# Kernel optimization log

Hardware: AMD Instinct MI355X
Metric: run time of the kernel (lower is better)

The kernel has to match this reference:

```python
import jax, jax.numpy as jnp
import numpy as np

NEG_SLOPE = 0.2  # PyG GATv2Conv default


def with_self_loops(edge_index, n):
    loop = jnp.arange(n, dtype=edge_index.dtype)
    src = jnp.concatenate([edge_index[0], loop])
    dst = jnp.concatenate([edge_index[1], loop])
    return src, dst


def gatv2(x, src, dst, Wl, bl, Wr, br, att, bias):
    """PyG GATv2Conv (eval mode, concat=True, add_self_loops done by caller).
    x: [N, F_in]; att: [H, C]. Returns [N, H*C]."""
    N = x.shape[0]
    H, C = att.shape
    xl = (x @ Wl + bl).reshape(N, H, C)  # lin_l(x): source-side transform
    xr = (x @ Wr + br).reshape(N, H, C)  # lin_r(x): target-side transform
    s = jax.nn.leaky_relu(xl[src] + xr[dst], NEG_SLOPE)      # [E,H,C]
    logit = jnp.einsum('ehc,hc->eh', s, att)                 # [E,H]
    m = jax.ops.segment_max(logit, dst, num_segments=N)      # stable softmax per target
    e = jnp.exp(logit - m[dst])
    den = jax.ops.segment_sum(e, dst, num_segments=N)
    alpha = e / (den[dst] + 1e-16)                           # [E,H]
    out = jax.ops.segment_sum(alpha[:, :, None] * xl[src], dst, num_segments=N)
    return out.reshape(N, H * C) + bias


def setup_inputs() -> dict:
    N, E = 20000, 320000        # agent nodes / edges
    M, EM = 40000, 400000       # lane nodes / edges
    B, L = 64, 50               # focal agents, centerline length
    SEQ, INC, HID, HEADS, OUT = 50, 2, 32, 4, 60
    H4 = HID * HEADS
    key = jax.random.key(0)
    ks = list(jax.random.split(key, 48))
    kit = iter(ks)

    def p(shape):
        return jax.random.normal(next(kit), shape, jnp.float32) * 0.05

    inp = {
        'x': jax.random.normal(next(kit), (N, SEQ, INC), jnp.float32),
        'edge_index': jax.random.randint(next(kit), (2, E), 0, N),
        'lane_x': jax.random.normal(next(kit), (M, 2), jnp.float32),
        'lane_edge_index': jax.random.randint(next(kit), (2, EM), 0, M),
        'batch': jnp.sort(jax.random.randint(next(kit), (N,), 0, B)),
        'focal_idx': jax.random.randint(next(kit), (B,), 0, N),
        'centerlines': jax.random.normal(next(kit), (B, L, 2), jnp.float32),
        # agent embedding
        'ae_W': p((SEQ * INC, HID)), 'ae_b': p((HID,)),
        # agent subgraph conv1 / conv2
        'a1_Wl': p((HID, H4)), 'a1_bl': p((H4,)), 'a1_Wr': p((HID, H4)), 'a1_br': p((H4,)), 'a1_att': p((HEADS, HID)), 'a1_b': p((H4,)),
        'a2_Wl': p((H4, H4)), 'a2_bl': p((H4,)), 'a2_Wr': p((H4, H4)), 'a2_br': p((H4,)), 'a2_att': p((HEADS, HID)), 'a2_b': p((H4,)),
        # map embedding + map subgraph
        'me_W': p((2, HID)), 'me_b': p((HID,)),
        'm1_Wl': p((HID, H4)), 'm1_bl': p((H4,)), 'm1_Wr': p((HID, H4)), 'm1_br': p((H4,)), 'm1_att': p((HEADS, HID)), 'm1_b': p((H4,)),
        'm2_Wl': p((H4, H4)), 'm2_bl': p((H4,)), 'm2_Wr': p((H4, H4)), 'm2_br': p((H4,)), 'm2_att': p((HEADS, HID)), 'm2_b': p((H4,)),
        # centerline processor
        'cl_W': p((2, HID)), 'cl_b': p((HID,)),
        # global graph (heads=1)
        'g_Wl': p((H4, HID)), 'g_bl': p((HID,)), 'g_Wr': p((H4, HID)), 'g_br': p((HID,)), 'g_att': p((1, HID)), 'g_b': p((HID,)),
        # output head
        'fc_W': p((2 * HID, OUT)), 'fc_b': p((OUT,)),
    }
    return inp


def reference(x, edge_index, lane_x, lane_edge_index, batch, focal_idx, centerlines,
              ae_W, ae_b,
              a1_Wl, a1_bl, a1_Wr, a1_br, a1_att, a1_b,
              a2_Wl, a2_bl, a2_Wr, a2_br, a2_att, a2_b,
              me_W, me_b,
              m1_Wl, m1_bl, m1_Wr, m1_br, m1_att, m1_b,
              m2_Wl, m2_bl, m2_Wr, m2_br, m2_att, m2_b,
              cl_W, cl_b,
              g_Wl, g_bl, g_Wr, g_br, g_att, g_b,
              fc_W, fc_b):
    N = x.shape[0]
    M = lane_x.shape[0]
    # agent branch
    agent_x = jax.nn.relu(x.reshape(N, -1) @ ae_W + ae_b)
    a_src, a_dst = with_self_loops(edge_index, N)
    h = jax.nn.relu(gatv2(agent_x, a_src, a_dst, a1_Wl, a1_bl, a1_Wr, a1_br, a1_att, a1_b))
    agent_features = jax.nn.relu(gatv2(h, a_src, a_dst, a2_Wl, a2_bl, a2_Wr, a2_br, a2_att, a2_b))  # [N,128]
    # map branch (output unused downstream in original, computed for faithfulness)
    map_x = jax.nn.relu(lane_x @ me_W + me_b)
    m_src, m_dst = with_self_loops(lane_edge_index, M)
    hm = jax.nn.relu(gatv2(map_x, m_src, m_dst, m1_Wl, m1_bl, m1_Wr, m1_br, m1_att, m1_b))
    map_features = jax.nn.relu(gatv2(hm, m_src, m_dst, m2_Wl, m2_bl, m2_Wr, m2_br, m2_att, m2_b))
    _ = map_features  # global_mean_pool results are dead code in the original forward
    # global graph over agent features (heads=1)
    global_features = jax.nn.relu(gatv2(agent_features, a_src, a_dst, g_Wl, g_bl, g_Wr, g_br, g_att, g_b))  # [N,32]
    focal = global_features[focal_idx]  # [B,32]
    # centerlines: per-polyline mean then linear (no relu, as in original)
    cl_feat = jnp.mean(centerlines, axis=1) @ cl_W + cl_b  # [B,32]
    combined = jnp.concatenate([focal, cl_feat], axis=1)
    return combined @ fc_W + fc_b
```

## Files before the change

### kernel.cpp

```cpp
#include <hip/hip_runtime.h>
#include <hip/hip_bf16.h>
#include <hip/hip_fp16.h>
#include <math.h>

typedef __hip_bfloat16 bf16;
#define NEG_SLOPE 0.2f

typedef _Float16 f16x8 __attribute__((ext_vector_type(8)));
typedef float f32x4 __attribute__((ext_vector_type(4)));

__global__ void k_detect_zero(const unsigned short* __restrict__ x, int* __restrict__ flag,
                              int* __restrict__ zbase, int n) {
    for (int i = blockIdx.x * blockDim.x + threadIdx.x; i < n; i += gridDim.x * blockDim.x)
        zbase[i] = 0;
    if (blockIdx.x == 0) {
        __shared__ int cnt;
        if (threadIdx.x == 0) cnt = 0;
        __syncthreads();
        int local = 0;
        for (int i = threadIdx.x; i < 2048; i += blockDim.x) {
            unsigned short w = x[2 * i];
            int e = (w >> 7) & 0xFF;
            if (e >= 0x90) local++;
        }
        atomicAdd(&cnt, local);
        __syncthreads();
        if (threadIdx.x == 0) flag[0] = (cnt > 100) ? 1 : 0;
    }
}

#define NSEG 25
struct Seg { const void* src; int n; int off; };
struct Tab { Seg s[NSEG]; };

__device__ __forceinline__ float ldconv(const void* src, int i, int f32mode) {
    return f32mode ? ((const float*)src)[i]
                   : __bfloat162float(((const bf16*)src)[i]);
}

__global__ void k_convert(Tab tab, float* __restrict__ dst, const int* __restrict__ flag,
                          const int* __restrict__ dstArr, int E, int N,
                          int* __restrict__ deg, int* __restrict__ rank,
                          const void* a2WlS, const void* a2WrS,
                          const void* gWlS, const void* gWrS,
                          __half* __restrict__ a2Wlt, __half* __restrict__ a2Wrt,
                          __half* __restrict__ gWlt, __half* __restrict__ gWrt) {
    int f32mode = flag[0];
    int gid = blockIdx.x * blockDim.x + threadIdx.x;
    int gsz = gridDim.x * blockDim.x;
    for (int s = 0; s < NSEG; s++) {
        Seg sg = tab.s[s];
        for (int i = gid; i < sg.n; i += gsz) {
            dst[sg.off + i] = ldconv(sg.src, i, f32mode);
        }
    }
    for (int i = gid; i < 128 * 128; i += gsz) {
        int k = i >> 7, j = i & 127;
        a2Wlt[(size_t)j * 128 + k] = __float2half(ldconv(a2WlS, i, f32mode));
        a2Wrt[(size_t)j * 128 + k] = __float2half(ldconv(a2WrS, i, f32mode));
    }
    for (int i = gid; i < 128 * 32; i += gsz) {
        int k = i >> 5, j = i & 31;
        gWlt[(size_t)j * 128 + k] = __float2half(ldconv(gWlS, i, f32mode));
        gWrt[(size_t)j * 128 + k] = __float2half(ldconv(gWrS, i, f32mode));
    }
    int EA = E + N;
    for (int e = gid; e < EA; e += gsz) {
        int d = (e < E) ? dstArr[e] : (e - E);
        rank[e] = atomicAdd(&deg[d], 1);
    }
}

__launch_bounds__(1024)
__global__ void k_scans(const int* __restrict__ deg, int* __restrict__ offs, int n) {
    __shared__ int ws[16];
    __shared__ int stot_s;
    __shared__ int carry_s;
    int t = threadIdx.x;
    if (t == 0) carry_s = 0;
    int lane = t & 63, wid = t >> 6;
    int nt = (n + 1023) >> 10;
    int vnext = (t < n) ? deg[t] : 0;
    for (int tile = 0; tile < nt; tile++) {
        int i = tile * 1024 + t;
        int v = vnext;
        int inx = i + 1024;
        vnext = (tile + 1 < nt && inx < n) ? deg[inx] : 0;
        int x = v;
        #pragma unroll
        for (int o = 1; o < 64; o <<= 1) {
            int y = __shfl_up(x, o);
            if (lane >= o) x += y;
        }
        if (lane == 63) ws[wid] = x;
        __syncthreads();
        if (wid == 0) {
            int w = (lane < 16) ? ws[lane] : 0;
            int s = w;
            #pragma unroll
            for (int o = 1; o < 16; o <<= 1) {
                int y = __shfl_up(s, o);
                if (lane >= o) s += y;
            }
            if (lane < 16) ws[lane] = s - w;
            if (lane == 15) stot_s = s;
        }
        __syncthreads();
        int cprev = carry_s;
        if (i < n) offs[i] = cprev + ws[wid] + x - v;
        __syncthreads();
        if (t == 0) carry_s = cprev + stot_s;
        __syncthreads();
    }
    if (t == 0) offs[n] = carry_s;
}

__launch_bounds__(256)
__global__ void k_fill_embedlin(const int* __restrict__ srcArr, const int* __restrict__ dstArr,
                                int E, int N, const int* __restrict__ offs,
                                const int* __restrict__ rank, int* __restrict__ csr,
                                const void* __restrict__ xraw, const int* __restrict__ flag,
                                const float* __restrict__ aeW, const float* __restrict__ aeb,
                                const float* __restrict__ Wl, const float* __restrict__ bl,
                                const float* __restrict__ Wr, const float* __restrict__ br,
                                __half* __restrict__ outl, float* __restrict__ outr,
                                int EB) {
    __shared__ float xs[100 * 36];
    __shared__ float axs[32 * 36];
    if (blockIdx.x >= EB) {
        int e = (blockIdx.x - EB) * 256 + threadIdx.x;
        int EA = E + N;
        if (e >= EA) return;
        int d, s;
        if (e < E) { d = dstArr[e]; s = srcArr[e]; } else { d = s = e - E; }
        csr[offs[d] + rank[e]] = s;
        return;
    }
    constexpr int NTP = 36;
    int t = threadIdx.x, nb = blockIdx.x * 32;
    if (flag[0]) {
        const float4* x4 = (const float4*)xraw;
        for (int idx = t; idx < 32 * 25; idx += 256) {
            int node = idx / 25, k4 = idx % 25;
            float4 v = x4[(size_t)(nb + node) * 25 + k4];
            xs[(k4 * 4 + 0) * NTP + node] = v.x;
            xs[(k4 * 4 + 1) * NTP + node] = v.y;
            xs[(k4 * 4 + 2) * NTP + node] = v.z;
            xs[(k4 * 4 + 3) * NTP + node] = v.w;
        }
    } else {
        const ushort4* xu = (const ushort4*)xraw;
        for (int idx = t; idx < 32 * 25; idx += 256) {
            int node = idx / 25, k4 = idx % 25;
            ushort4 u = xu[(size_t)(nb + node) * 25 + k4];
            xs[(k4 * 4 + 0) * NTP + node] = __uint_as_float((unsigned)u.x << 16);
            xs[(k4 * 4 + 1) * NTP + node] = __uint_as_float((unsigned)u.y << 16);
            xs[(k4 * 4 + 2) * NTP + node] = __uint_as_float((unsigned)u.z << 16);
            xs[(k4 * 4 + 3) * NTP + node] = __uint_as_float((unsigned)u.w << 16);
        }
    }
    __syncthreads();
    {
        int j = t & 31, g0 = t >> 5;
        float a0 = 0.f, a1 = 0.f, a2 = 0.f, a3 = 0.f;
        #pragma unroll 10
        for (int k = 0; k < 100; k++) {
            float w = aeW[k * 32 + j];
            const float4 xv = *(const float4*)&xs[k * NTP + g0 * 4];
            a0 += w * xv.x; a1 += w * xv.y; a2 += w * xv.z; a3 += w * xv.w;
        }
        float bj = aeb[j];
        axs[j * NTP + g0 * 4 + 0] = fmaxf(a0 + bj, 0.f);
        axs[j * NTP + g0 * 4 + 1] = fmaxf(a1 + bj, 0.f);
        axs[j * NTP + g0 * 4 + 2] = fmaxf(a2 + bj, 0.f);
        axs[j * NTP + g0 * 4 + 3] = fmaxf(a3 + bj, 0.f);
    }
    __syncthreads();
    {
        int j = t & 63, g0 = t >> 6;
        float aL0[2][4], aL1[2][4], aR0[2][4], aR1[2][4];
        #pragma unroll
        for (int g = 0; g < 2; g++)
            #pragma unroll
            for (int c = 0; c < 4; c++) { aL0[g][c]=0.f; aL1[g][c]=0.f; aR0[g][c]=0.f; aR1[g][c]=0.f; }
        #pragma unroll 4
        for (int k = 0; k < 32; k++) {
            float wl0 = Wl[k * 128 + j];
            float wl1 = Wl[k * 128 + j + 64];
            float wr0 = Wr[k * 128 + j];
            float wr1 = Wr[k * 128 + j + 64];
            #pragma unroll
            for (int g = 0; g < 2; g++) {
                const float4 xv = *(const float4*)&axs[k * NTP + (g0 + g * 4) * 4];
                aL0[g][0] += wl0 * xv.x; aL0[g][1] += wl0 * xv.y; aL0[g][2] += wl0 * xv.z; aL0[g][3] += wl0 * xv.w;
                aL1[g][0] += wl1 * xv.x; aL1[g][1] += wl1 * xv.y; aL1[g][2] += wl1 * xv.z; aL1[g][3] += wl1 * xv.w;
                aR0[g][0] += wr0 * xv.x; aR0[g][1] += wr0 * xv.y; aR0[g][2] += wr0 * xv.z; aR0[g][3] += wr0 * xv.w;
                aR1[g][0] += wr1 * xv.x; aR1[g][1] += wr1 * xv.y; aR1[g][2] += wr1 * xv.z; aR1[g][3] += wr1 * xv.w;
            }
        }
        float bl0 = bl[j], bl1 = bl[j + 64], br0 = br[j], br1 = br[j + 64];
        #pragma unroll
        for (int g = 0; g < 2; g++) {
            int n0 = nb + (g0 + g * 4) * 4;
            #pragma unroll
            for (int c = 0; c < 4; c++) {
                size_t row = (size_t)(n0 + c) * 128;
                outl[row + j]      = __float2half(aL0[g][c] + bl0);
                outl[row + j + 64] = __float2half(aL1[g][c] + bl1);
                outr[row + j]      = aR0[g][c] + br0;
                outr[row + j + 64] = aR1[g][c] + br1;
            }
        }
    }
}

__device__ __forceinline__ void gat_proc(float4 raw, bool valid,
                                         const float* xrd, const float* av,
                                         float* acc, float& sm) {
    const __half2* h = (const __half2*)&raw;
    float v[8];
    float2 f;
    f = __half22float2(h[0]); v[0] = f.x; v[1] = f.y;
    f = __half22float2(h[1]); v[2] = f.x; v[3] = f.y;
    f = __half22float2(h[2]); v[4] = f.x; v[5] = f.y;
    f = __half22float2(h[3]); v[6] = f.x; v[7] = f.y;
    float p = 0.f;
    #pragma unroll
    for (int c = 0; c < 8; c++) {
        float u = v[c] + xrd[c];
        u = (u > 0.f) ? u : NEG_SLOPE * u;
        p += u * av[c];
    }
    p += __shfl_xor(p, 1);
    p += __shfl_xor(p, 2);
    p += __shfl_xor(p, 4);
    p += __shfl_xor(p, 8);
    float w = __expf(fminf(p, 80.f));
    if (!valid) w = 0.f;
    sm += w;
    #pragma unroll
    for (int c = 0; c < 8; c++) acc[c] += w * v[c];
}

__device__ __forceinline__ void gat16_to_lds(__half* xsh,
                                             const __half* __restrict__ xl,
                                             const float* xrp,
                                             const float* __restrict__ att,
                                             const int* __restrict__ offs,
                                             const int* __restrict__ csr,
                                             const float* __restrict__ bias,
                                             int d, int node) {
    int t = threadIdx.x;
    int lane = t & 63;
    int sub = lane & 15;
    int lb = lane & 48;
    float av[8];
    {
        const float4* t4 = (const float4*)(att + sub * 8);
        float4 c = t4[0], e = t4[1];
        av[0]=c.x; av[1]=c.y; av[2]=c.z; av[3]=c.w;
        av[4]=e.x; av[5]=e.y; av[6]=e.z; av[7]=e.w;
    }
    bool ok = d >= 0;
    int i0 = ok ? offs[d] : 0;
    int i1 = ok ? offs[d + 1] : 0;
    int cnt = i1 - i0;

    float xrd[8];
    #pragma unroll
    for (int c = 0; c < 8; c++) xrd[c] = 0.f;
    if (ok) {
        const float4* p4 = (const float4*)(xrp + sub * 8);
        float4 a = p4[0], b = p4[1];
        xrd[0]=a.x; xrd[1]=a.y; xrd[2]=a.z; xrd[3]=a.w;
        xrd[4]=b.x; xrd[5]=b.y; xrd[6]=b.z; xrd[7]=b.w;
    }
    float acc[8];
    #pragma unroll
    for (int c = 0; c < 8; c++) acc[c] = 0.f;
    float sm = 0.f;

    int myv = (sub < cnt) ? csr[i0 + sub] : 0;
    for (int c0 = 0; c0 < cnt; c0 += 16) {
        int myv_nxt = (c0 + 16 + sub < cnt) ? csr[i0 + c0 + 16 + sub] : 0;
        int rem = min(cnt - c0, 16);
        for (int k = 0; k < rem; k += 4) {
            int s0 = __shfl(myv, lb + k + 0);
            int s1 = __shfl(myv, lb + k + 1);
            int s2 = __shfl(myv, lb + k + 2);
            int s3 = __shfl(myv, lb + k + 3);
            float4 r0 = *(const float4*)(xl + (size_t)s0 * 128 + sub * 8);
            float4 r1 = *(const float4*)(xl + (size_t)s1 * 128 + sub * 8);
            float4 r2 = *(const float4*)(xl + (size_t)s2 * 128 + sub * 8);
            float4 r3 = *(const float4*)(xl + (size_t)s3 * 128 + sub * 8);
            gat_proc(r0, true,        xrd, av, acc, sm);
            gat_proc(r1, k + 1 < rem, xrd, av, acc, sm);
            gat_proc(r2, k + 2 < rem, xrd, av, acc, sm);
            gat_proc(r3, k + 3 < rem, xrd, av, acc, sm);
        }
        myv = myv_nxt;
    }

    int ch = sub * 8;
    if (ok) {
        float inv = 1.f / (sm + 1e-16f);
        #pragma unroll
        for (int c = 0; c < 8; c += 2) {
            __half2 hv;
            hv.x = __float2half(fmaxf(acc[c]     * inv + bias[ch + c],     0.f));
            hv.y = __float2half(fmaxf(acc[c + 1] * inv + bias[ch + c + 1], 0.f));
            *(__half2*)&xsh[node * 136 + ch + c] = hv;
        }
    } else {
        #pragma unroll
        for (int c = 0; c < 8; c += 2)
            *(__half2*)&xsh[node * 136 + ch + c] = __half2{__half(0.f), __half(0.f)};
    }
}

__launch_bounds__(256)
__global__ void k_gatlin(const __half* __restrict__ xl, const float* __restrict__ xr,
                         const float* __restrict__ att,
                         const int* __restrict__ offs, const int* __restrict__ csr,
                         const float* __restrict__ bias,
                         const __half* __restrict__ Wlt, const float* __restrict__ bl,
                         __half* __restrict__ outl, __half* __restrict__ outf1, int N,
                         const int* __restrict__ focal, int B,
                         int* __restrict__ L, int* __restrict__ Lcnt, int GT) {
    if (blockIdx.x >= GT) {
        int t = threadIdx.x;
        if (t < B) {
            int f = focal[t];
            int j0 = offs[f], j1 = offs[f + 1];
            int base = atomicAdd(Lcnt, j1 - j0);
            for (int j = j0; j < j1; j++) L[base + (j - j0)] = csr[j];
        }
        return;
    }
    __shared__ __align__(16) __half xsh[16 * 136];
    int nb = blockIdx.x * 16;
    int t = threadIdx.x;
    int lane = t & 63, wv = t >> 6;
    int quad = lane >> 4, n16 = lane & 15;
    {
        int node = wv * 4 + quad;
        int dd = nb + node;
        bool okd = dd < N;
        const float* xrp = xr + (size_t)(okd ? dd : 0) * 128;
        gat16_to_lds(xsh, xl, xrp, att, offs, csr, bias, okd ? dd : -1, node);
    }
    __syncthreads();

    {
        int node = t >> 4, ch = (t & 15) * 8;
        if (nb + node < N)
            *(f16x8*)&outf1[(size_t)(nb + node) * 128 + ch] =
                *(const f16x8*)&xsh[node * 136 + ch];
    }

    f16x8 a[4];
    #pragma unroll
    for (int kt = 0; kt < 4; kt++)
        a[kt] = *(const f16x8*)&xsh[n16 * 136 + kt * 32 + quad * 8];

    int j0 = wv * 32;
    f32x4 aL0 = {0.f,0.f,0.f,0.f}, aL1 = {0.f,0.f,0.f,0.f};
    #pragma unroll
    for (int kt = 0; kt < 4; kt++) {
        int ko = kt * 32 + quad * 8;
        f16x8 b0 = *(const f16x8*)&Wlt[(size_t)(j0 + n16) * 128 + ko];
        f16x8 b1 = *(const f16x8*)&Wlt[(size_t)(j0 + 16 + n16) * 128 + ko];
        aL0 = __builtin_amdgcn_mfma_f32_16x16x32_f16(a[kt], b0, aL0, 0, 0, 0);
        aL1 = __builtin_amdgcn_mfma_f32_16x16x32_f16(a[kt], b1, aL1, 0, 0, 0);
    }
    float blj0 = bl[j0 + n16], blj1 = bl[j0 + 16 + n16];
    #pragma unroll
    for (int r = 0; r < 4; r++) {
        int node = quad * 4 + r;
        if (nb + node >= N) continue;
        size_t row = (size_t)(nb + node) * 128;
        outl[row + j0 + n16]      = __float2half(aL0[r] + blj0);
        outl[row + j0 + 16 + n16] = __float2half(aL1[r] + blj1);
    }
}

__launch_bounds__(256)
__global__ void k_gatling(const __half* __restrict__ xl,
                          const __half* __restrict__ hf1,
                          const __half* __restrict__ Wrt2,
                          const float* __restrict__ br2,
                          const float* __restrict__ att,
                          const int* __restrict__ offs, const int* __restrict__ csr,
                          const float* __restrict__ bias,
                          const __half* __restrict__ Wlt, const float* __restrict__ bl,
                          const __half* __restrict__ Wrt, const float* __restrict__ br,
                          __half* __restrict__ outl, float* __restrict__ outr,
                          const int* __restrict__ L, const int* __restrict__ Lcnt) {
    __shared__ __align__(16) __half xsh[16 * 136];
    __shared__ __align__(16) float xr2[16 * 132];
    int total = *Lcnt;
    int t = threadIdx.x;
    int lane = t & 63, wv = t >> 6;
    int quad = lane >> 4, n16 = lane & 15;

    for (int tile = blockIdx.x; tile * 16 < total; tile += gridDim.x) {
        if (tile != (int)blockIdx.x) __syncthreads();
        {
            int ia = tile * 16 + n16;
            int da = (ia < total) ? L[ia] : -1;
            f16x8 af[4];
            if (da >= 0) {
                #pragma unroll
                for (int kt = 0; kt < 4; kt++)
                    af[kt] = *(const f16x8*)&hf1[(size_t)da * 128 + kt * 32 + quad * 8];
            } else {
                #pragma unroll
                for (int kt = 0; kt < 4; kt++)
                    #pragma unroll
                    for (int c = 0; c < 8; c++) af[kt][c] = (_Float16)0;
            }
            f32x4 ar0 = {0.f,0.f,0.f,0.f}, ar1 = {0.f,0.f,0.f,0.f};
            #pragma unroll
            for (int kt = 0; kt < 4; kt++) {
                int ko = kt * 32 + quad * 8;
                f16x8 b0 = *(const f16x8*)&Wrt2[(size_t)(wv * 32 + n16) * 128 + ko];
                f16x8 b1 = *(const f16x8*)&Wrt2[(size_t)(wv * 32 + 16 + n16) * 128 + ko];
                ar0 = __builtin_amdgcn_mfma_f32_16x16x32_f16(af[kt], b0, ar0, 0, 0, 0);
                ar1 = __builtin_amdgcn_mfma_f32_16x16x32_f16(af[kt], b1, ar1, 0, 0, 0);
            }
            int c0 = wv * 32 + n16, c1 = wv * 32 + 16 + n16;
            float bb0 = br2[c0], bb1 = br2[c1];
            #pragma unroll
            for (int r = 0; r < 4; r++) {
                int row = quad * 4 + r;
                xr2[row * 132 + c0] = ar0[r] + bb0;
                xr2[row * 132 + c1] = ar1[r] + bb1;
            }
        }
        __syncthreads();
        int node = wv * 4 + quad;
        int idx = tile * 16 + node;
        int d = (idx < total) ? L[idx] : -1;
        gat16_to_lds(xsh, xl, &xr2[node * 132], att, offs, csr, bias, d, node);
        __syncthreads();
        f16x8 a[4];
        #pragma unroll
        for (int kt = 0; kt < 4; kt++)
            a[kt] = *(const f16x8*)&xsh[n16 * 136 + kt * 32 + quad * 8];

        const __half* Wt = (wv < 2) ? Wlt : Wrt;
        int j0 = (wv & 1) * 16;
        f32x4 accv = {0.f,0.f,0.f,0.f};
        #pragma unroll
        for (int kt = 0; kt < 4; kt++) {
            f16x8 b = *(const f16x8*)&Wt[(size_t)(j0 + n16) * 128 + kt * 32 + quad * 8];
            accv = __builtin_amdgcn_mfma_f32_16x16x32_f16(a[kt], b, accv, 0, 0, 0);
        }
        float bj = ((wv < 2) ? bl : br)[j0 + n16];
        #pragma unroll
        for (int r = 0; r < 4; r++) {
            int nn = quad * 4 + r;
            int gidx = tile * 16 + nn;
            if (gidx >= total) continue;
            int gd = L[gidx];
            size_t row = (size_t)gd * 32;
            if (wv < 2) outl[row + j0 + n16] = __float2half(accv[r] + bj);
            else        outr[row + j0 + n16] = accv[r] + bj;
        }
    }
}

__launch_bounds__(64)
__global__ void k_tailf(const __half* __restrict__ xl, const float* __restrict__ xr,
                        const float* __restrict__ att,
                        const int* __restrict__ offs, const int* __restrict__ csr,
                        const float* __restrict__ gb, const int* __restrict__ focal,
                        const float* __restrict__ clf, const float* __restrict__ clW,
                        const float* __restrict__ clb, const float* __restrict__ fcW,
                        const float* __restrict__ fcb, void* __restrict__ out,
                        const int* __restrict__ flag) {
    __shared__ float comb[64];
    __shared__ float ssb[2];
    int b = blockIdx.x;
    int t = threadIdx.x;
    int d = focal[b];
    int grp = t >> 3, sub = t & 7;
    int i0 = offs[d], i1 = offs[d + 1];

    float xrd[4], av[4], acc[4];
    {
        float4 a = *(const float4*)(xr + (size_t)d * 32 + sub * 4);
        xrd[0]=a.x; xrd[1]=a.y; xrd[2]=a.z; xrd[3]=a.w;
        float4 c = *(const float4*)(att + sub * 4);
        av[0]=c.x; av[1]=c.y; av[2]=c.z; av[3]=c.w;
    }
    #pragma unroll
    for (int c = 0; c < 4; c++) acc[c] = 0.f;
    float sm = 0.f;

    for (int i = i0 + grp; i < i1; i += 8) {
        float2 raw = *(const float2*)(xl + (size_t)csr[i] * 32 + sub * 4);
        const __half2* h = (const __half2*)&raw;
        float v[4];
        float2 f;
        f = __half22float2(h[0]); v[0] = f.x; v[1] = f.y;
        f = __half22float2(h[1]); v[2] = f.x; v[3] = f.y;
        float p = 0.f;
        #pragma unroll
        for (int c = 0; c < 4; c++) {
            float u = v[c] + xrd[c];
            u = (u > 0.f) ? u : NEG_SLOPE * u;
            p += u * av[c];
        }
        p += __shfl_xor(p, 1);
        p += __shfl_xor(p, 2);
        p += __shfl_xor(p, 4);
        float w = __expf(fminf(p, 80.f));
        sm += w;
        #pragma unroll
        for (int c = 0; c < 4; c++) acc[c] += w * v[c];
    }
    sm += __shfl_xor(sm, 8); sm += __shfl_xor(sm, 16); sm += __shfl_xor(sm, 32);
    #pragma unroll
    for (int c = 0; c < 4; c++) {
        acc[c] += __shfl_xor(acc[c], 8);
        acc[c] += __shfl_xor(acc[c], 16);
        acc[c] += __shfl_xor(acc[c], 32);
    }
    if (grp == 0) {
        float inv = 1.f / (sm + 1e-16f);
        #pragma unroll
        for (int c = 0; c < 4; c++)
            comb[sub * 4 + c] = fmaxf(acc[c] * inv + gb[sub * 4 + c], 0.f);
    }
    if (t < 2) {
        float s = 0.f;
        for (int l = 0; l < 50; l++) s += clf[(size_t)b * 100 + l * 2 + t];
        ssb[t] = s / 50.f;
    }
    __syncthreads();
    if (t < 32) comb[32 + t] = ssb[0] * clW[t] + ssb[1] * clW[32 + t] + clb[t];
    __syncthreads();
    if (t < 60) {
        float a2 = fcb[t];
        #pragma unroll 16
        for (int k = 0; k < 64; k++) a2 += comb[k] * fcW[k * 60 + t];
        if (flag[0]) ((float*)out)[b * 60 + t] = a2;
        else ((bf16*)out)[b * 60 + t] = __float2bfloat16(a2);
    }
}

extern "C" void kernel_launch(void* const* d_in, const int* in_sizes, int n_in,
                              void* d_out, int out_size, void* d_ws, size_t ws_size,
                              hipStream_t stream) {
    const int* edge  = (const int*)d_in[1];
    const int* focal = (const int*)d_in[5];

    const int N = in_sizes[0] / 100;
    const int E = in_sizes[1] / 2;
    const int B = in_sizes[5];
    const int EA = E + N;
    const int* srcArr = edge;
    const int* dstArr = edge + E;

    const int idxs[NSEG] = {7,8,9,10,11,12,13,14,15,16,17,18,19,20,
                            35,36,37,38,39,40,41,42,43,44, 6};
    float* base = (float*)d_ws;
    int* flag = (int*)base;
    float* wf = base + 16;
    Tab tab;
    int off[NSEG];
    int o = 0;
    for (int i = 0; i < NSEG; i++) {
        tab.s[i].src = d_in[idxs[i]];
        tab.s[i].n   = in_sizes[idxs[i]];
        tab.s[i].off = o;
        off[i] = o;
        o += in_sizes[idxs[i]];
    }
    const float* aeW  = wf + off[0],  *aeb  = wf + off[1];
    const float* a1Wl = wf + off[2],  *a1bl = wf + off[3];
    const float* a1Wr = wf + off[4],  *a1br = wf + off[5];
    const float* a1att= wf + off[6],  *a1b  = wf + off[7];
    const float* a2bl = wf + off[9];
    const float* a2br = wf + off[11];
    const float* a2att= wf + off[12], *a2b  = wf + off[13];
    const float* clW  = wf + off[14], *clb  = wf + off[15];
    const float* gbl  = wf + off[17];
    const float* gbr  = wf + off[19];
    const float* gatt = wf + off[20], *gb   = wf + off[21];
    const float* fcW  = wf + off[22], *fcb  = wf + off[23];
    const float* clf  = wf + off[24];

    float* p = wf + o + ((4 - (o & 3)) & 3);
    size_t N128 = (size_t)N * 128;
    __half* hxl1 = (__half*)p;      p += (size_t)N * 64;
    float* fB1  = p;                p += N128;
    __half* hxl2 = (__half*)p;      p += (size_t)N * 64;
    __half* hf1  = (__half*)p;      p += (size_t)N * 64;
    int* deg    = (int*)p;
    int* st     = deg + N;
    int* offs   = st + 32;
    int* rank   = offs + N + 1;
    int* csr    = rank + EA;
    uintptr_t up = (uintptr_t)(csr + EA);
    up = (up + 15) & ~(uintptr_t)15;
    __half* a2Wlt = (__half*)up;
    __half* a2Wrt = a2Wlt + 16384;
    __half* gWlt  = a2Wrt + 16384;
    __half* gWrt  = gWlt + 4096;
    int* Lbuf = (int*)(gWrt + 4096);
    int* Lcnt = st + 30;

    const int EB = N / 32;
    const int FBLK = (EA + 255) / 256;
    const int GT = (N + 15) / 16;

    k_detect_zero<<<64, 256, 0, stream>>>((const unsigned short*)d_in[0], flag, deg, N + 32);
    k_convert<<<256, 256, 0, stream>>>(tab, wf, flag, dstArr, E, N, deg, rank,
                                       d_in[15], d_in[17], d_in[37], d_in[39],
                                       a2Wlt, a2Wrt, gWlt, gWrt);
    k_scans<<<1, 1024, 0, stream>>>(deg, offs, N);
    k_fill_embedlin<<<EB + FBLK, 256, 0, stream>>>(srcArr, dstArr, E, N, offs, rank, csr,
                                                   d_in[0], flag, aeW, aeb,
                                                   a1Wl, a1bl, a1Wr, a1br, hxl1, fB1, EB);
    k_gatlin<<<GT + 1, 256, 0, stream>>>(hxl1, fB1, a1att, offs, csr, a1b,
                                         a2Wlt, a2bl, hxl2, hf1, N,
                                         focal, B, Lbuf, Lcnt, GT);
    k_gatling<<<128, 256, 0, stream>>>(hxl2, hf1, a2Wrt, a2br, a2att, offs, csr, a2b,
                                       gWlt, gbl, gWrt, gbr, hxl1, fB1, Lbuf, Lcnt);
    k_tailf<<<B, 64, 0, stream>>>(hxl1, fB1, gatt, offs, csr, gb, focal,
                                  clf, clW, clb, fcW, fcb, d_out, flag);
}
```

Baseline: 256.7 us.

## Fuse degree scan into fill kernel with flag-based handoff to CSR blocks

The separate single-block scan kernel is removed. Block 0 of the fill/embed kernel now computes the degree prefix sum, reading four ints per thread, and publishes completion through a global release flag. The CSR-fill blocks spin on that flag while the embedding blocks run concurrently, so the serial scan overlaps useful work and one launch is saved. Zeroing moves to hipMemsetAsync and detection to a one-block kernel. The spin-wait depends on block 0 being scheduled before or alongside the waiting blocks, which risks deadlock if dispatch order or residency assumptions fail.

```diff
diff --git a/kernel.cpp b/kernel.cpp
--- a/kernel.cpp
+++ b/kernel.cpp
@@ -9,24 +9,19 @@
 typedef _Float16 f16x8 __attribute__((ext_vector_type(8)));
 typedef float f32x4 __attribute__((ext_vector_type(4)));
 
-__global__ void k_detect_zero(const unsigned short* __restrict__ x, int* __restrict__ flag,
-                              int* __restrict__ zbase, int n) {
-    for (int i = blockIdx.x * blockDim.x + threadIdx.x; i < n; i += gridDim.x * blockDim.x)
-        zbase[i] = 0;
-    if (blockIdx.x == 0) {
-        __shared__ int cnt;
-        if (threadIdx.x == 0) cnt = 0;
-        __syncthreads();
-        int local = 0;
-        for (int i = threadIdx.x; i < 2048; i += blockDim.x) {
-            unsigned short w = x[2 * i];
-            int e = (w >> 7) & 0xFF;
-            if (e >= 0x90) local++;
-        }
-        atomicAdd(&cnt, local);
-        __syncthreads();
-        if (threadIdx.x == 0) flag[0] = (cnt > 100) ? 1 : 0;
-    }
+__global__ void k_detect(const unsigned short* __restrict__ x, int* __restrict__ flag) {
+    __shared__ int cnt;
+    if (threadIdx.x == 0) cnt = 0;
+    __syncthreads();
+    int local = 0;
+    for (int i = threadIdx.x; i < 2048; i += blockDim.x) {
+        unsigned short w = x[2 * i];
+        int e = (w >> 7) & 0xFF;
+        if (e >= 0x90) local++;
+    }
+    atomicAdd(&cnt, local);
+    __syncthreads();
+    if (threadIdx.x == 0) flag[0] = (cnt > 100) ? 1 : 0;
 }
 
 #define NSEG 25
@@ -71,53 +66,10 @@
     }
 }
 
-__launch_bounds__(1024)
-__global__ void k_scans(const int* __restrict__ deg, int* __restrict__ offs, int n) {
-    __shared__ int ws[16];
-    __shared__ int stot_s;
-    __shared__ int carry_s;
-    int t = threadIdx.x;
-    if (t == 0) carry_s = 0;
-    int lane = t & 63, wid = t >> 6;
-    int nt = (n + 1023) >> 10;
-    int vnext = (t < n) ? deg[t] : 0;
-    for (int tile = 0; tile < nt; tile++) {
-        int i = tile * 1024 + t;
-        int v = vnext;
-        int inx = i + 1024;
-        vnext = (tile + 1 < nt && inx < n) ? deg[inx] : 0;
-        int x = v;
-        #pragma unroll
-        for (int o = 1; o < 64; o <<= 1) {
-            int y = __shfl_up(x, o);
-            if (lane >= o) x += y;
-        }
-        if (lane == 63) ws[wid] = x;
-        __syncthreads();
-        if (wid == 0) {
-            int w = (lane < 16) ? ws[lane] : 0;
-            int s = w;
-            #pragma unroll
-            for (int o = 1; o < 16; o <<= 1) {
-                int y = __shfl_up(s, o);
-                if (lane >= o) s += y;
-            }
-            if (lane < 16) ws[lane] = s - w;
-            if (lane == 15) stot_s = s;
-        }
-        __syncthreads();
-        int cprev = carry_s;
-        if (i < n) offs[i] = cprev + ws[wid] + x - v;
-        __syncthreads();
-        if (t == 0) carry_s = cprev + stot_s;
-        __syncthreads();
-    }
-    if (t == 0) offs[n] = carry_s;
-}
-
 __launch_bounds__(256)
 __global__ void k_fill_embedlin(const int* __restrict__ srcArr, const int* __restrict__ dstArr,
-                                int E, int N, const int* __restrict__ offs,
+                                int E, int N, const int* __restrict__ deg,
+                                int* __restrict__ offs, int* __restrict__ scanflag,
                                 const int* __restrict__ rank, int* __restrict__ csr,
                                 const void* __restrict__ xraw, const int* __restrict__ flag,
                                 const float* __restrict__ aeW, const float* __restrict__ aeb,
@@ -125,10 +77,62 @@
                                 const float* __restrict__ Wr, const float* __restrict__ br,
                                 __half* __restrict__ outl, float* __restrict__ outr,
                                 int EB) {
-    __shared__ float xs[100 * 36];
-    __shared__ float axs[32 * 36];
-    if (blockIdx.x >= EB) {
-        int e = (blockIdx.x - EB) * 256 + threadIdx.x;
+    if (blockIdx.x == 0) {
+        __shared__ int wsum[4];
+        __shared__ int carry_s;
+        int t = threadIdx.x;
+        int lane = t & 63, wid = t >> 6;
+        if (t == 0) carry_s = 0;
+        __syncthreads();
+        int nt = (N + 1023) >> 10;
+        for (int tile = 0; tile < nt; tile++) {
+            int i0 = tile * 1024 + t * 4;
+            int4 v = {0, 0, 0, 0};
+            if (i0 + 3 < N) v = *(const int4*)&deg[i0];
+            else {
+                if (i0     < N) v.x = deg[i0];
+                if (i0 + 1 < N) v.y = deg[i0 + 1];
+                if (i0 + 2 < N) v.z = deg[i0 + 2];
+                if (i0 + 3 < N) v.w = deg[i0 + 3];
+            }
+            int s4 = v.x + v.y + v.z + v.w;
+            int x = s4;
+            #pragma unroll
+            for (int o = 1; o < 64; o <<= 1) {
+                int y = __shfl_up(x, o);
+                if (lane >= o) x += y;
+            }
+            if (lane == 63) wsum[wid] = x;
+            __syncthreads();
+            int wpre = 0;
+            #pragma unroll
+            for (int w = 0; w < 4; w++) if (w < wid) wpre += wsum[w];
+            int tot = wsum[0] + wsum[1] + wsum[2] + wsum[3];
+            int cprev = carry_s;
+            int pre = cprev + wpre + (x - s4);
+            if (i0     < N) offs[i0]     = pre;
+            if (i0 + 1 < N) offs[i0 + 1] = pre + v.x;
+            if (i0 + 2 < N) offs[i0 + 2] = pre + v.x + v.y;
+            if (i0 + 3 < N) offs[i0 + 3] = pre + v.x + v.y + v.z;
+            __syncthreads();
+            if (t == 0) carry_s = cprev + tot;
+        }
+        __syncthreads();
+        if (t == 0) {
+            offs[N] = carry_s;
+            __threadfence();
+            __hip_atomic_store(scanflag, 1, __ATOMIC_RELEASE, __HIP_MEMORY_SCOPE_AGENT);
+        }
+        return;
+    }
+    if (blockIdx.x > EB) {
+        if (threadIdx.x == 0) {
+            while (__hip_atomic_load(scanflag, __ATOMIC_ACQUIRE,
+                                     __HIP_MEMORY_SCOPE_AGENT) == 0)
+                __builtin_amdgcn_s_sleep(8);
+        }
+        __syncthreads();
+        int e = (blockIdx.x - EB - 1) * 256 + threadIdx.x;
         int EA = E + N;
         if (e >= EA) return;
         int d, s;
@@ -136,8 +140,10 @@
         csr[offs[d] + rank[e]] = s;
         return;
     }
+    __shared__ float xs[100 * 36];
+    __shared__ float axs[32 * 36];
     constexpr int NTP = 36;
-    int t = threadIdx.x, nb = blockIdx.x * 32;
+    int t = threadIdx.x, nb = (blockIdx.x - 1) * 32;
     if (flag[0]) {
         const float4* x4 = (const float4*)xraw;
         for (int idx = t; idx < 32 * 25; idx += 256) {
@@ -611,19 +617,22 @@
     __half* gWrt  = gWlt + 4096;
     int* Lbuf = (int*)(gWrt + 4096);
     int* Lcnt = st + 30;
+    int* scanflag = st + 31;
 
     const int EB = N / 32;
     const int FBLK = (EA + 255) / 256;
     const int GT = (N + 15) / 16;
 
-    k_detect_zero<<<64, 256, 0, stream>>>((const unsigned short*)d_in[0], flag, deg, N + 32);
+    hipMemsetAsync(deg, 0, (size_t)(N + 32) * sizeof(int), stream);
+    k_detect<<<1, 256, 0, stream>>>((const unsigned short*)d_in[0], flag);
     k_convert<<<256, 256, 0, stream>>>(tab, wf, flag, dstArr, E, N, deg, rank,
                                        d_in[15], d_in[17], d_in[37], d_in[39],
                                        a2Wlt, a2Wrt, gWlt, gWrt);
-    k_scans<<<1, 1024, 0, stream>>>(deg, offs, N);
-    k_fill_embedlin<<<EB + FBLK, 256, 0, stream>>>(srcArr, dstArr, E, N, offs, rank, csr,
-                                                   d_in[0], flag, aeW, aeb,
-                                                   a1Wl, a1bl, a1Wr, a1br, hxl1, fB1, EB);
+    k_fill_embedlin<<<1 + EB + FBLK, 256, 0, stream>>>(srcArr, dstArr, E, N, deg,
+                                                       offs, scanflag, rank, csr,
+                                                       d_in[0], flag, aeW, aeb,
+                                                       a1Wl, a1bl, a1Wr, a1br,
+                                                       hxl1, fB1, EB);
     k_gatlin<<<GT + 1, 256, 0, stream>>>(hxl1, fB1, a1att, offs, csr, a1b,
                                          a2Wlt, a2bl, hxl2, hf1, N,
                                          focal, B, Lbuf, Lcnt, GT);
```

After: 535.0 us. +108.4%, slower.
